# Kernel tuning notes

Measured on AMD Instinct MI355X. Metric: run time of the kernel, lower is better.

The kernel has to match this reference:

```python
import jax, jax.numpy as jnp
import numpy as np

EMBED_DIM = 1024
NUM_HEADS = 16
HEAD_DIM = EMBED_DIM // NUM_HEADS


def setup_inputs() -> dict:
    key = jax.random.key(0)
    ks = jax.random.split(key, 11)
    B, T, C = 2, 2048, EMBED_DIM
    s = 1.0 / np.sqrt(C)  # ~ torch Linear init scale
    inp = {
        "q": jax.random.normal(ks[0], (B, T, C), jnp.float32),
        "k": jax.random.normal(ks[1], (B, T, C), jnp.float32),
        "v": jax.random.normal(ks[2], (B, T, C), jnp.float32),
        "Wq": jax.random.normal(ks[3], (C, C), jnp.float32) * s,
        "bq": jax.random.normal(ks[4], (C,), jnp.float32) * s,
        "Wk": jax.random.normal(ks[5], (C, C), jnp.float32) * s,
        "bk": jax.random.normal(ks[6], (C,), jnp.float32) * s,
        "Wv": jax.random.normal(ks[7], (C, C), jnp.float32) * s,
        "bv": jax.random.normal(ks[8], (C,), jnp.float32) * s,
        "Wo": jax.random.normal(ks[9], (C, C), jnp.float32) * s,
        "bo": jax.random.normal(ks[10], (C,), jnp.float32) * s,
    }
    return inp


def _split_heads(x):
    B, T, C = x.shape
    return x.reshape(B, T, NUM_HEADS, HEAD_DIM).transpose(0, 2, 1, 3)  # [B,H,T,Dh]


def reference(q, k, v, Wq, bq, Wk, bk, Wv, bv, Wo, bo):
    B, Tq, C = q.shape
    # torch Linear: y = x @ W.T + b
    qh = _split_heads(q @ Wq.T + bq)
    kh = _split_heads(k @ Wk.T + bk)
    vh = _split_heads(v @ Wv.T + bv)
    scale = 1.0 / np.sqrt(HEAD_DIM).astype(np.float32)
    logits = jnp.einsum("bhqd,bhkd->bhqk", qh, kh) * scale
    attn = jax.nn.softmax(logits, axis=-1)
    out = jnp.einsum("bhqk,bhkd->bhqd", attn, vh)
    out = out.transpose(0, 2, 1, 3).reshape(B, Tq, C)
    return out @ Wo.T + bo
```

## Files before the change

### kernel.cpp

```cpp
#include <hip/hip_runtime.h>
#include <stdint.h>

#define T_SEQ 2048
#define CDIM 1024
#define NHEAD 16
#define HDIM 64
#define MROWS 4096

typedef unsigned short u16;
typedef __attribute__((ext_vector_type(8))) short bf16x8;
typedef __attribute__((ext_vector_type(4))) float f32x4;
typedef __attribute__((ext_vector_type(16))) float f32x16;
typedef __attribute__((ext_vector_type(4))) unsigned short u16x4;
typedef __attribute__((ext_vector_type(4))) unsigned int uint4v;

#if __has_builtin(__builtin_amdgcn_exp2f)
#define EXP2(x) __builtin_amdgcn_exp2f(x)
#else
#define EXP2(x) exp2f(x)
#endif

__device__ __forceinline__ u16 f2bf(float f) {
  unsigned u = __builtin_bit_cast(unsigned, f);
  u += 0x7fffu + ((u >> 16) & 1u);
  return (u16)(u >> 16);
}

__device__ __forceinline__ unsigned cvt_pk_bf16(float lo, float hi) {
  unsigned r;
  asm("v_cvt_pk_bf16_f32 %0, %1, %2" : "=v"(r) : "v"(lo), "v"(hi));
  return r;
}

__device__ __forceinline__ void pls(unsigned &a, unsigned &b) {
  asm("v_permlane32_swap_b32 %0, %1" : "+v"(a), "+v"(b));
}

__device__ __forceinline__ void gll16(const void* g, void* l) {
  __builtin_amdgcn_global_load_lds((__attribute__((address_space(1))) void*)(g),
                                   (__attribute__((address_space(3))) void*)(l),
                                   16, 0, 0);
}

__device__ __forceinline__ void wg_barrier() {
  asm volatile("" ::: "memory");
  __builtin_amdgcn_s_barrier();
  asm volatile("" ::: "memory");
}

#define WAIT_VM(N) do { __builtin_amdgcn_s_waitcnt(0xF00 | 0x70 | (N)); \
                        asm volatile("" ::: "memory"); } while (0)

__global__ __launch_bounds__(256)
void cvt_all(const float* __restrict__ q, const float* __restrict__ k, const float* __restrict__ v,
             const float* __restrict__ wq, const float* __restrict__ wk,
             const float* __restrict__ wv, const float* __restrict__ wo,
             u16* __restrict__ qb, u16* __restrict__ kb, u16* __restrict__ vb,
             u16* __restrict__ wqb, u16* __restrict__ wkb, u16* __restrict__ wvb, u16* __restrict__ wob) {
  int b = blockIdx.x;
  const float* src; u16* dst; int base;
  if (b < 1536) {
    int s = b >> 9;
    src = (s == 0) ? q : (s == 1) ? k : v;
    dst = (s == 0) ? qb : (s == 1) ? kb : vb;
    base = (b & 511) * 2048;
  } else {
    int s = (b - 1536) >> 7;
    src = (s == 0) ? wq : (s == 1) ? wk : (s == 2) ? wv : wo;
    dst = (s == 0) ? wqb : (s == 1) ? wkb : (s == 2) ? wvb : wob;
    base = ((b - 1536) & 127) * 2048;
  }
#pragma unroll
  for (int j = 0; j < 8; ++j) {
    int i = base + j * 256 + threadIdx.x;
    float4 a = ((const float4*)src)[i];
    u16x4 o = { f2bf(a.x), f2bf(a.y), f2bf(a.z), f2bf(a.w) };
    ((u16x4*)dst)[i] = o;
  }
}


__device__ __forceinline__ void gemm_stage(const u16* Ag, const u16* Bg, u16* Ad, u16* Bd) {
#pragma unroll
  for (int c = 0; c < 4; ++c) {
    gll16(Ag + c * 32 * CDIM, Ad + c * 2048);
    gll16(Bg + c * 32 * CDIM, Bd + c * 2048);
  }
}

__device__ __forceinline__ void gemm_compute(const u16* As, const u16* Bs,
                                             f32x4 (&acc)[4][4],
                                             int wr, int wc, int lg, int lr) {
#pragma unroll
  for (int kk = 0; kk < 2; ++kk) {
    bf16x8 af[4], bfr[4];
#pragma unroll
    for (int f = 0; f < 4; ++f) {
      int ra = wr * 64 + f * 16 + lr;
      af[f]  = *(const bf16x8*)((const char*)As + ra * 128 + ((lg * 16 + kk * 64) ^ ((ra & 7) << 4)));
      int rb = wc * 64 + f * 16 + lr;
      bfr[f] = *(const bf16x8*)((const char*)Bs + rb * 128 + ((lg * 16 + kk * 64) ^ ((rb & 7) << 4)));
    }
#pragma unroll
    for (int i = 0; i < 4; ++i)
#pragma unroll
      for (int j = 0; j < 4; ++j)
        acc[i][j] = __builtin_amdgcn_mfma_f32_16x16x32_bf16(af[i], bfr[j], acc[i][j], 0, 0, 0);
  }
}

#define GEMM_KLOOP(As, Bs, Ad0, Bd0, Ad1, Bd1)                                 \
  gemm_stage(Ag, Bg, Ad0, Bd0);                                                \
  _Pragma("unroll 1")                                                          \
  for (int kt = 0; kt < 16; ++kt) {                                            \
    wg_barrier();                                                              \
    int nt = (kt + 1 < 16) ? kt + 1 : 15;                                      \
    if (kt & 1) gemm_stage(Ag + nt * 64, Bg + nt * 64, Ad0, Bd0);              \
    else        gemm_stage(Ag + nt * 64, Bg + nt * 64, Ad1, Bd1);              \
    WAIT_VM(8);                                                                \
    wg_barrier();                                                              \
    gemm_compute((kt & 1) ? As[1] : As[0], (kt & 1) ? Bs[1] : Bs[0],           \
                 acc, wr, wc, lg, lr);                                         \
  }

__global__ __launch_bounds__(256)
void gemm_qkv(const u16* __restrict__ A0, const u16* __restrict__ A1, const u16* __restrict__ A2,
              const u16* __restrict__ W0, const u16* __restrict__ W1, const u16* __restrict__ W2,
              const float* __restrict__ b0, const float* __restrict__ b1, const float* __restrict__ b2,
              u16* __restrict__ o0, u16* __restrict__ o1, u16* __restrict__ o2,
              float qscale) {
  __shared__ u16 As[2][128 * 64];
  __shared__ u16 Bs[2][128 * 64];
  const int z = blockIdx.z;
  const u16* A   = (z == 0) ? A0 : (z == 1) ? A1 : A2;
  const u16* Bw  = (z == 0) ? W0 : (z == 1) ? W1 : W2;
  const float* bias = (z == 0) ? b0 : (z == 1) ? b1 : b2;
  u16* outp = (z == 0) ? o0 : (z == 1) ? o1 : o2;
  const float scale = (z == 0) ? qscale : 1.0f;

  const int m0 = blockIdx.y * 128;
  const int n0 = blockIdx.x * 128;
  const int tid = threadIdx.x;
  const int w = tid >> 6, l = tid & 63;
  const int wr = w >> 1, wc = w & 1;
  const int lg = l >> 4, lr = l & 15;

  const int row0 = tid >> 3, slot0 = tid & 7;
  const int so = (slot0 ^ (row0 & 7)) << 3;
  const u16* Ag = A  + ((size_t)(m0 + row0)) * CDIM + so;
  const u16* Bg = Bw + ((size_t)(n0 + row0)) * CDIM + so;
  u16* Ad0 = As[0] + w * 512;  u16* Bd0 = Bs[0] + w * 512;
  u16* Ad1 = As[1] + w * 512;  u16* Bd1 = Bs[1] + w * 512;

  f32x4 acc[4][4] = {};

  GEMM_KLOOP(As, Bs, Ad0, Bd0, Ad1, Bd1)

#pragma unroll
  for (int fj = 0; fj < 4; ++fj) {
    int col = n0 + wc * 64 + fj * 16 + lr;
    float bv = bias[col];
    int h = col >> 6, d = col & 63;
#pragma unroll
    for (int fi = 0; fi < 4; ++fi) {
#pragma unroll
      for (int i = 0; i < 4; ++i) {
        int row = m0 + wr * 64 + fi * 16 + lg * 4 + i;
        float val = (acc[fi][fj][i] + bv) * scale;
        int b = row >> 11, t = row & 2047;
        if (z < 2)
          outp[(((size_t)(b * NHEAD + h)) * T_SEQ + t) * HDIM + d] = f2bf(val);
        else
          outp[(((size_t)(b * NHEAD + h)) * HDIM + d) * T_SEQ + t] = f2bf(val);
      }
    }
  }
}

__global__ __launch_bounds__(256)
void gemm_bt0(const u16* __restrict__ A, const u16* __restrict__ Bw,
              const float* __restrict__ bias, float* __restrict__ outp) {
  __shared__ u16 As[2][128 * 64];
  __shared__ u16 Bs[2][128 * 64];
  const int m0 = blockIdx.y * 128;
  const int n0 = blockIdx.x * 128;
  const int tid = threadIdx.x;
  const int w = tid >> 6, l = tid & 63;
  const int wr = w >> 1, wc = w & 1;
  const int lg = l >> 4, lr = l & 15;

  const int row0 = tid >> 3, slot0 = tid & 7;
  const int so = (slot0 ^ (row0 & 7)) << 3;
  const u16* Ag = A  + ((size_t)(m0 + row0)) * CDIM + so;
  const u16* Bg = Bw + ((size_t)(n0 + row0)) * CDIM + so;
  u16* Ad0 = As[0] + w * 512;  u16* Bd0 = Bs[0] + w * 512;
  u16* Ad1 = As[1] + w * 512;  u16* Bd1 = Bs[1] + w * 512;

  f32x4 acc[4][4] = {};

  GEMM_KLOOP(As, Bs, Ad0, Bd0, Ad1, Bd1)

#pragma unroll
  for (int fj = 0; fj < 4; ++fj) {
    int col = n0 + wc * 64 + fj * 16 + lr;
    float bv = bias[col];
#pragma unroll
    for (int fi = 0; fi < 4; ++fi) {
#pragma unroll
      for (int i = 0; i < 4; ++i) {
        int row = m0 + wr * 64 + fi * 16 + lg * 4 + i;
        outp[(size_t)row * CDIM + col] = acc[fi][fj][i] + bv;
      }
    }
  }
}


__device__ __forceinline__ void attn_stage(const u16* Kg, const u16* Vg, u16* Kd, u16* Vd) {
#pragma unroll
  for (int c = 0; c < 2; ++c) {
    gll16(Kg + c * 32 * HDIM,  Kd + c * 2048);
    gll16(Vg + c * 32 * T_SEQ, Vd + c * 2048);
  }
}

__device__ __forceinline__ void attn_tile(const char* Kb, const char* Vb,
                                          const bf16x8 (&qf)[4],
                                          f32x16 (&acc)[2], f32x4& lsum, float& m_run,
                                          int lo5, int hi, int swz) {
  f32x16 s[2] = {};
  const int colK = 16 * hi;
  __builtin_amdgcn_s_setprio(1);
#pragma unroll
  for (int st = 0; st < 4; ++st) {
    bf16x8 k0 = *(const bf16x8*)(Kb + lo5 * 128        + ((32 * st + colK) ^ swz));
    bf16x8 k1 = *(const bf16x8*)(Kb + (lo5 + 32) * 128 + ((32 * st + colK) ^ swz));
    s[0] = __builtin_amdgcn_mfma_f32_32x32x16_bf16(k0, qf[st], s[0], 0, 0, 0);
    s[1] = __builtin_amdgcn_mfma_f32_32x32x16_bf16(k1, qf[st], s[1], 0, 0, 0);
  }
  __builtin_amdgcn_s_setprio(0);

  float t[8];
#pragma unroll
  for (int i = 0; i < 8; ++i)
    t[i] = fmaxf(fmaxf(s[0][2 * i], s[0][2 * i + 1]), fmaxf(s[1][2 * i], s[1][2 * i + 1]));
  float u0 = fmaxf(fmaxf(t[0], t[1]), fmaxf(t[2], t[3]));
  float u1 = fmaxf(fmaxf(t[4], t[5]), fmaxf(t[6], t[7]));
  float tl = fmaxf(u0, u1);
  if (!__all(tl <= m_run + 8.f)) {
    float tmax = fmaxf(tl, __shfl_xor(tl, 32));
    float m_new = fmaxf(m_run, tmax);
    float alpha = EXP2(m_run - m_new);
    lsum[0] *= alpha; lsum[1] *= alpha; lsum[2] *= alpha; lsum[3] *= alpha;
#pragma unroll
    for (int i = 0; i < 16; ++i) { acc[0][i] *= alpha; acc[1][i] *= alpha; }
    m_run = m_new;
  }

  unsigned pg[2][8];
#pragma unroll
  for (int g = 0; g < 8; ++g) {
    float a0 = EXP2(s[0][2 * g] - m_run), b0 = EXP2(s[0][2 * g + 1] - m_run);
    float a1 = EXP2(s[1][2 * g] - m_run), b1 = EXP2(s[1][2 * g + 1] - m_run);
    lsum[g & 3] += (a0 + b0) + (a1 + b1);
    pg[0][g] = cvt_pk_bf16(a0, b0);
    pg[1][g] = cvt_pk_bf16(a1, b1);
  }

  bf16x8 pb[4];
#pragma unroll
  for (int sub = 0; sub < 2; ++sub)
#pragma unroll
    for (int ks = 0; ks < 2; ++ks) {
      unsigned w0 = pg[sub][4 * ks + 0], w1 = pg[sub][4 * ks + 1];
      unsigned w2 = pg[sub][4 * ks + 2], w3 = pg[sub][4 * ks + 3];
      pls(w0, w2); pls(w1, w3);
      uint4v tt = { w0, w1, w2, w3 };
      pb[2 * sub + ks] = __builtin_bit_cast(bf16x8, tt);
    }

  __builtin_amdgcn_s_setprio(1);
#pragma unroll
  for (int ks = 0; ks < 4; ++ks) {
    bf16x8 v0 = *(const bf16x8*)(Vb + lo5 * 128        + ((32 * ks + colK) ^ swz));
    bf16x8 v1 = *(const bf16x8*)(Vb + (lo5 + 32) * 128 + ((32 * ks + colK) ^ swz));
    acc[0] = __builtin_amdgcn_mfma_f32_32x32x16_bf16(v0, pb[ks], acc[0], 0, 0, 0);
    acc[1] = __builtin_amdgcn_mfma_f32_32x32x16_bf16(v1, pb[ks], acc[1], 0, 0, 0);
  }
  __builtin_amdgcn_s_setprio(0);
}

__global__ __launch_bounds__(256)
void attn_fused(const u16* __restrict__ Qh, const u16* __restrict__ Kh,
                const u16* __restrict__ Vt, u16* __restrict__ Ao) {
  __shared__ u16 Ks[2][64 * 64];
  __shared__ u16 Vs[2][64 * 64];
  const int bh = blockIdx.y;
  const int q0 = blockIdx.x * 128;
  const int tid = threadIdx.x;
  const int w = tid >> 6, l = tid & 63;
  const int lo5 = l & 31, hi = l >> 5;
  const int swz = (l & 7) << 4;

  const u16* qptr = Qh + ((size_t)bh * T_SEQ + q0 + w * 32 + lo5) * HDIM + hi * 8;
  bf16x8 qf[4];
#pragma unroll
  for (int s = 0; s < 4; ++s) qf[s] = *(const bf16x8*)(qptr + 16 * s);

  const int row0 = tid >> 3, slot0 = tid & 7;
  const int so = (slot0 ^ (row0 & 7)) << 3;
  const u16* Kg = Kh + ((size_t)bh * T_SEQ + row0) * HDIM + so;
  const u16* Vg = Vt + ((size_t)bh * HDIM + row0) * T_SEQ + so;
  u16* Kd0 = Ks[0] + w * 512;  u16* Vd0 = Vs[0] + w * 512;
  u16* Kd1 = Ks[1] + w * 512;  u16* Vd1 = Vs[1] + w * 512;

  f32x16 acc[2] = {};
  f32x4 lsum = {};
  float m_run = -1e30f;

  attn_stage(Kg, Vg, Kd0, Vd0);
#pragma unroll 1
  for (int kv = 0; kv < 32; ++kv) {
    wg_barrier();
    int nt = (kv + 1 < 32) ? kv + 1 : 31;
    if (kv & 1) attn_stage(Kg + (size_t)nt * 64 * HDIM, Vg + nt * 64, Kd0, Vd0);
    else        attn_stage(Kg + (size_t)nt * 64 * HDIM, Vg + nt * 64, Kd1, Vd1);
    WAIT_VM(4);
    wg_barrier();
    attn_tile((const char*)(kv & 1 ? Ks[1] : Ks[0]),
              (const char*)(kv & 1 ? Vs[1] : Vs[0]),
              qf, acc, lsum, m_run, lo5, hi, swz);
  }

  float ls = (lsum[0] + lsum[1]) + (lsum[2] + lsum[3]);
  ls += __shfl_xor(ls, 32);
  float inv = 1.f / ls;

  wg_barrier();
  char* os = (char*)(Ks[0]) + w * 4096;
#pragma unroll
  for (int dsub = 0; dsub < 2; ++dsub)
#pragma unroll
    for (int gg = 0; gg < 4; ++gg) {
      unsigned wa = cvt_pk_bf16(acc[dsub][4 * gg + 0] * inv, acc[dsub][4 * gg + 1] * inv);
      unsigned wb = cvt_pk_bf16(acc[dsub][4 * gg + 2] * inv, acc[dsub][4 * gg + 3] * inv);
      uint2 wv = { wa, wb };
      int byte = lo5 * 128 + (((32 * dsub + 8 * gg + 4 * hi) * 2) ^ swz);
      *(uint2*)(os + byte) = wv;
    }
  int b = bh >> 4, h = bh & 15;
#pragma unroll
  for (int c = 0; c < 4; ++c) {
    int qq = 8 * c + (l >> 3);
    uint4v ov = *(const uint4v*)(os + qq * 128 + ((16 * (l & 7)) ^ ((qq & 7) << 4)));
    *(uint4v*)(Ao + ((size_t)(b * T_SEQ + q0 + w * 32 + qq)) * CDIM + h * HDIM + (l & 7) * 8) = ov;
  }
}

extern "C" void kernel_launch(void* const* d_in, const int* in_sizes, int n_in,
                              void* d_out, int out_size, void* d_ws, size_t ws_size,
                              hipStream_t stream) {
  const float* q  = (const float*)d_in[0];
  const float* k  = (const float*)d_in[1];
  const float* v  = (const float*)d_in[2];
  const float* Wq = (const float*)d_in[3];
  const float* bq = (const float*)d_in[4];
  const float* Wk = (const float*)d_in[5];
  const float* bk = (const float*)d_in[6];
  const float* Wv = (const float*)d_in[7];
  const float* bv = (const float*)d_in[8];
  const float* Wo = (const float*)d_in[9];
  const float* bo = (const float*)d_in[10];

  char* ws = (char*)d_ws;
  size_t off = 0;
  auto alloc = [&](size_t n) { void* p = ws + off; off += (n + 255) & ~(size_t)255; return p; };
  const size_t NX = (size_t)MROWS * CDIM;
  const size_t NW = (size_t)CDIM * CDIM;
  u16* qb  = (u16*)alloc(NX * 2);
  u16* kb  = (u16*)alloc(NX * 2);
  u16* vb  = (u16*)alloc(NX * 2);
  u16* Wqb = (u16*)alloc(NW * 2);
  u16* Wkb = (u16*)alloc(NW * 2);
  u16* Wvb = (u16*)alloc(NW * 2);
  u16* Wob = (u16*)alloc(NW * 2);
  u16* Qhp = (u16*)alloc(NX * 2);
  u16* Khp = (u16*)alloc(NX * 2);
  u16* Vtp = (u16*)alloc(NX * 2);
  u16* Aop = (u16*)alloc(NX * 2);

  cvt_all<<<2048, 256, 0, stream>>>(q, k, v, Wq, Wk, Wv, Wo,
                                    qb, kb, vb, Wqb, Wkb, Wvb, Wob);

  const float qscale = 0.18033688011112042f;
  gemm_qkv<<<dim3(CDIM / 128, MROWS / 128, 3), 256, 0, stream>>>(
      qb, kb, vb, Wqb, Wkb, Wvb, bq, bk, bv, Qhp, Khp, Vtp, qscale);

  attn_fused<<<dim3(T_SEQ / 128, 32), 256, 0, stream>>>(Qhp, Khp, Vtp, Aop);

  gemm_bt0<<<dim3(CDIM / 128, MROWS / 128), 256, 0, stream>>>(Aop, Wob, bo, (float*)d_out);

  (void)in_sizes; (void)n_in; (void)out_size; (void)ws_size;
}
```

Before: 136.0 us.

## Split attention KV loop across two wave groups with cross-group softmax merge

The attention kernel now launches 512 threads per block, and two groups of four waves each process alternating KV tiles for the same 128 queries. This halves the serial KV iteration count per wave. At the end the partial max, sum and accumulators are merged through shared memory. The change doubles the LDS staging buffers to 64KB and adds an epilogue exchange with extra barriers, which may lower occupancy.

```diff
diff --git a/kernel.cpp b/kernel.cpp
--- a/kernel.cpp
+++ b/kernel.cpp
@@ -216,14 +216,6 @@
 }
 
 
-__device__ __forceinline__ void attn_stage(const u16* Kg, const u16* Vg, u16* Kd, u16* Vd) {
-#pragma unroll
-  for (int c = 0; c < 2; ++c) {
-    gll16(Kg + c * 32 * HDIM,  Kd + c * 2048);
-    gll16(Vg + c * 32 * T_SEQ, Vd + c * 2048);
-  }
-}
-
 __device__ __forceinline__ void attn_tile(const char* Kb, const char* Vb,
                                           const bf16x8 (&qf)[4],
                                           f32x16 (&acc)[2], f32x4& lsum, float& m_run,
@@ -290,70 +282,122 @@
   __builtin_amdgcn_s_setprio(0);
 }
 
-__global__ __launch_bounds__(256)
+__global__ __launch_bounds__(512, 4)
 void attn_fused(const u16* __restrict__ Qh, const u16* __restrict__ Kh,
                 const u16* __restrict__ Vt, u16* __restrict__ Ao) {
-  __shared__ u16 Ks[2][64 * 64];
-  __shared__ u16 Vs[2][64 * 64];
+  __shared__ u16 Ks[2][2][64 * 64];
+  __shared__ u16 Vs[2][2][64 * 64];
   const int bh = blockIdx.y;
   const int q0 = blockIdx.x * 128;
   const int tid = threadIdx.x;
   const int w = tid >> 6, l = tid & 63;
+  const int grp = w >> 2, wq = w & 3;
   const int lo5 = l & 31, hi = l >> 5;
   const int swz = (l & 7) << 4;
 
-  const u16* qptr = Qh + ((size_t)bh * T_SEQ + q0 + w * 32 + lo5) * HDIM + hi * 8;
+  const u16* qptr = Qh + ((size_t)bh * T_SEQ + q0 + wq * 32 + lo5) * HDIM + hi * 8;
   bf16x8 qf[4];
 #pragma unroll
   for (int s = 0; s < 4; ++s) qf[s] = *(const bf16x8*)(qptr + 16 * s);
 
-  const int row0 = tid >> 3, slot0 = tid & 7;
-  const int so = (slot0 ^ (row0 & 7)) << 3;
-  const u16* Kg = Kh + ((size_t)bh * T_SEQ + row0) * HDIM + so;
-  const u16* Vg = Vt + ((size_t)bh * HDIM + row0) * T_SEQ + so;
-  u16* Kd0 = Ks[0] + w * 512;  u16* Vd0 = Vs[0] + w * 512;
-  u16* Kd1 = Ks[1] + w * 512;  u16* Vd1 = Vs[1] + w * 512;
+  const int par = w & 1, sub = (w >> 1) & 1;
+  const int row8 = l >> 3, slot = l & 7;
+
+  auto stage = [&](int step, int db) {
+    int t = 2 * step + par;
+    if (grp == 0) {
+      u16* dst = Ks[db][par] + sub * 32 * 64;
+      const u16* src = Kh + ((size_t)bh * T_SEQ + (size_t)t * 64 + sub * 32 + row8) * HDIM
+                          + ((slot ^ row8) << 3);
+#pragma unroll
+      for (int j = 0; j < 4; ++j)
+        gll16(src + j * 8 * HDIM, dst + j * 8 * 64);
+    } else {
+      u16* dst = Vs[db][par] + sub * 32 * 64;
+      const u16* src = Vt + ((size_t)bh * HDIM + sub * 32 + row8) * T_SEQ + (size_t)t * 64
+                          + ((slot ^ row8) << 3);
+#pragma unroll
+      for (int j = 0; j < 4; ++j)
+        gll16(src + (size_t)j * 8 * T_SEQ, dst + j * 8 * 64);
+    }
+  };
 
   f32x16 acc[2] = {};
   f32x4 lsum = {};
   float m_run = -1e30f;
 
-  attn_stage(Kg, Vg, Kd0, Vd0);
+  stage(0, 0);
 #pragma unroll 1
-  for (int kv = 0; kv < 32; ++kv) {
+  for (int s = 0; s < 16; ++s) {
     wg_barrier();
-    int nt = (kv + 1 < 32) ? kv + 1 : 31;
-    if (kv & 1) attn_stage(Kg + (size_t)nt * 64 * HDIM, Vg + nt * 64, Kd0, Vd0);
-    else        attn_stage(Kg + (size_t)nt * 64 * HDIM, Vg + nt * 64, Kd1, Vd1);
+    int ns = (s + 1 < 16) ? s + 1 : 15;
+    stage(ns, (s + 1) & 1);
     WAIT_VM(4);
     wg_barrier();
-    attn_tile((const char*)(kv & 1 ? Ks[1] : Ks[0]),
-              (const char*)(kv & 1 ? Vs[1] : Vs[0]),
+    attn_tile((const char*)Ks[s & 1][grp], (const char*)Vs[s & 1][grp],
               qf, acc, lsum, m_run, lo5, hi, swz);
   }
 
   float ls = (lsum[0] + lsum[1]) + (lsum[2] + lsum[3]);
   ls += __shfl_xor(ls, 32);
-  float inv = 1.f / ls;
 
   wg_barrier();
-  char* os = (char*)(Ks[0]) + w * 4096;
-#pragma unroll
-  for (int dsub = 0; dsub < 2; ++dsub)
-#pragma unroll
-    for (int gg = 0; gg < 4; ++gg) {
-      unsigned wa = cvt_pk_bf16(acc[dsub][4 * gg + 0] * inv, acc[dsub][4 * gg + 1] * inv);
-      unsigned wb = cvt_pk_bf16(acc[dsub][4 * gg + 2] * inv, acc[dsub][4 * gg + 3] * inv);
-      uint2 wv = { wa, wb };
-      int byte = lo5 * 128 + (((32 * dsub + 8 * gg + 4 * hi) * 2) ^ swz);
-      *(uint2*)(os + byte) = wv;
-    }
-  int b = bh >> 4, h = bh & 15;
-#pragma unroll
-  for (int c = 0; c < 4; ++c) {
-    int qq = 8 * c + (l >> 3);
-    uint4v ov = *(const uint4v*)(os + qq * 128 + ((16 * (l & 7)) ^ ((qq & 7) << 4)));
-    *(uint4v*)(Ao + ((size_t)(b * T_SEQ + q0 + w * 32 + qq)) * CDIM + h * HDIM + (l & 7) * 8) = ov;
+  float* ex = (float*)&Ks[0][0][0];
+  if (hi == 0) {
+    ex[w * 32 + lo5] = m_run;
+    ex[256 + w * 32 + lo5] = ls;
+  }
+  wg_barrier();
+  const int ow = w ^ 4;
+  float m_oth = ex[ow * 32 + lo5];
+  float l_oth = ex[256 + ow * 32 + lo5];
+  float m_fin = fmaxf(m_run, m_oth);
+  float fs = EXP2(m_run - m_fin);
+  float fo = EXP2(m_oth - m_fin);
+  float l_tot = ls * fs + l_oth * fo;
+#pragma unroll
+  for (int i = 0; i < 16; ++i) { acc[0][i] *= fs; acc[1][i] *= fs; }
+
+  float* ab = (float*)&Vs[0][0][0];
+  if (grp == 1) {
+#pragma unroll
+    for (int du = 0; du < 2; ++du)
+#pragma unroll
+      for (int c = 0; c < 4; ++c) {
+        f32x4 t4 = { acc[du][4 * c + 0], acc[du][4 * c + 1],
+                     acc[du][4 * c + 2], acc[du][4 * c + 3] };
+        *(f32x4*)(ab + ((wq * 64 + l) * 32 + du * 16 + c * 4)) = t4;
+      }
+  }
+  wg_barrier();
+  if (grp == 0) {
+#pragma unroll
+    for (int du = 0; du < 2; ++du)
+#pragma unroll
+      for (int c = 0; c < 4; ++c) {
+        f32x4 t4 = *(const f32x4*)(ab + ((wq * 64 + l) * 32 + du * 16 + c * 4));
+        acc[du][4 * c + 0] += t4[0]; acc[du][4 * c + 1] += t4[1];
+        acc[du][4 * c + 2] += t4[2]; acc[du][4 * c + 3] += t4[3];
+      }
+    float inv = 1.f / l_tot;
+    char* os = (char*)&Ks[0][0][0] + 4096 + wq * 4096;
+#pragma unroll
+    for (int dsub = 0; dsub < 2; ++dsub)
+#pragma unroll
+      for (int gg = 0; gg < 4; ++gg) {
+        unsigned wa = cvt_pk_bf16(acc[dsub][4 * gg + 0] * inv, acc[dsub][4 * gg + 1] * inv);
+        unsigned wb = cvt_pk_bf16(acc[dsub][4 * gg + 2] * inv, acc[dsub][4 * gg + 3] * inv);
+        uint2 wv = { wa, wb };
+        int byte = lo5 * 128 + (((32 * dsub + 8 * gg + 4 * hi) * 2) ^ swz);
+        *(uint2*)(os + byte) = wv;
+      }
+    int b = bh >> 4, h = bh & 15;
+#pragma unroll
+    for (int c = 0; c < 4; ++c) {
+      int qq = 8 * c + (l >> 3);
+      uint4v ov = *(const uint4v*)(os + qq * 128 + ((16 * (l & 7)) ^ ((qq & 7) << 4)));
+      *(uint4v*)(Ao + ((size_t)(b * T_SEQ + q0 + wq * 32 + qq)) * CDIM + h * HDIM + (l & 7) * 8) = ov;
+    }
   }
 }
 
@@ -396,7 +440,7 @@
   gemm_qkv<<<dim3(CDIM / 128, MROWS / 128, 3), 256, 0, stream>>>(
       qb, kb, vb, Wqb, Wkb, Wvb, bq, bk, bv, Qhp, Khp, Vtp, qscale);
 
-  attn_fused<<<dim3(T_SEQ / 128, 32), 256, 0, stream>>>(Qhp, Khp, Vtp, Aop);
+  attn_fused<<<dim3(T_SEQ / 128, 32), 512, 0, stream>>>(Qhp, Khp, Vtp, Aop);
 
   gemm_bt0<<<dim3(CDIM / 128, MROWS / 128), 256, 0, stream>>>(Aop, Wob, bo, (float*)d_out);
 
```

Result: faster. 129.2 us (-5.0%).

## Split attention KV range across two blocks and combine partials

Applied to the files above, without the earlier changes.

Splits each attention block's 32 KV tiles into two halves handled by separate blocks (grid z=2), writing partial normalized outputs plus running max and sum, then adds a combine kernel that merges the two halves with softmax rescaling. This doubles the attention grid from 512 to 1024 blocks to improve CU occupancy on the 256-CU device, and sets launch bounds to allow 4 blocks per CU. It also changes the staging so each wave loads either K or V. The cost is an extra kernel launch, extra global traffic for the partials, and partial outputs rounded to bf16 before the combine.

```diff
diff --git a/kernel.cpp b/kernel.cpp
--- a/kernel.cpp
+++ b/kernel.cpp
@@ -24,6 +24,10 @@
   unsigned u = __builtin_bit_cast(unsigned, f);
   u += 0x7fffu + ((u >> 16) & 1u);
   return (u16)(u >> 16);
+}
+
+__device__ __forceinline__ float bf2f(unsigned hw) {
+  return __builtin_bit_cast(float, hw << 16);
 }
 
 __device__ __forceinline__ unsigned cvt_pk_bf16(float lo, float hi) {
@@ -216,14 +220,6 @@
 }
 
 
-__device__ __forceinline__ void attn_stage(const u16* Kg, const u16* Vg, u16* Kd, u16* Vd) {
-#pragma unroll
-  for (int c = 0; c < 2; ++c) {
-    gll16(Kg + c * 32 * HDIM,  Kd + c * 2048);
-    gll16(Vg + c * 32 * T_SEQ, Vd + c * 2048);
-  }
-}
-
 __device__ __forceinline__ void attn_tile(const char* Kb, const char* Vb,
                                           const bf16x8 (&qf)[4],
                                           f32x16 (&acc)[2], f32x4& lsum, float& m_run,
@@ -290,13 +286,15 @@
   __builtin_amdgcn_s_setprio(0);
 }
 
-__global__ __launch_bounds__(256)
+__global__ __launch_bounds__(256, 4)
 void attn_fused(const u16* __restrict__ Qh, const u16* __restrict__ Kh,
-                const u16* __restrict__ Vt, u16* __restrict__ Ao) {
+                const u16* __restrict__ Vt, u16* __restrict__ Op,
+                float2* __restrict__ ml) {
   __shared__ u16 Ks[2][64 * 64];
   __shared__ u16 Vs[2][64 * 64];
   const int bh = blockIdx.y;
   const int q0 = blockIdx.x * 128;
+  const int half = blockIdx.z;
   const int tid = threadIdx.x;
   const int w = tid >> 6, l = tid & 63;
   const int lo5 = l & 31, hi = l >> 5;
@@ -307,28 +305,42 @@
 #pragma unroll
   for (int s = 0; s < 4; ++s) qf[s] = *(const bf16x8*)(qptr + 16 * s);
 
-  const int row0 = tid >> 3, slot0 = tid & 7;
-  const int so = (slot0 ^ (row0 & 7)) << 3;
-  const u16* Kg = Kh + ((size_t)bh * T_SEQ + row0) * HDIM + so;
-  const u16* Vg = Vt + ((size_t)bh * HDIM + row0) * T_SEQ + so;
-  u16* Kd0 = Ks[0] + w * 512;  u16* Vd0 = Vs[0] + w * 512;
-  u16* Kd1 = Ks[1] + w * 512;  u16* Vd1 = Vs[1] + w * 512;
+  const int srow = (w & 1) * 32 + (l >> 3);
+  const int soff = ((l & 7) ^ ((l >> 3) & 7)) << 3;
+  const u16* Kgs = Kh + ((size_t)bh * T_SEQ + srow) * HDIM + soff;
+  const u16* Vgs = Vt + ((size_t)bh * HDIM + srow) * T_SEQ + soff;
+  const int isV = w >> 1;
+
+  auto stage = [&](int t, int db) {
+    if (!isV) {
+      u16* dst = Ks[db] + (w & 1) * 32 * 64;
+      const u16* src = Kgs + (size_t)t * 64 * HDIM;
+#pragma unroll
+      for (int j = 0; j < 4; ++j)
+        gll16(src + j * 8 * HDIM, dst + j * 8 * 64);
+    } else {
+      u16* dst = Vs[db] + (w & 1) * 32 * 64;
+      const u16* src = Vgs + t * 64;
+#pragma unroll
+      for (int j = 0; j < 4; ++j)
+        gll16(src + (size_t)j * 8 * T_SEQ, dst + j * 8 * 64);
+    }
+  };
 
   f32x16 acc[2] = {};
   f32x4 lsum = {};
   float m_run = -1e30f;
-
-  attn_stage(Kg, Vg, Kd0, Vd0);
+  const int tb = half * 16;
+
+  stage(tb, 0);
 #pragma unroll 1
-  for (int kv = 0; kv < 32; ++kv) {
+  for (int s = 0; s < 16; ++s) {
     wg_barrier();
-    int nt = (kv + 1 < 32) ? kv + 1 : 31;
-    if (kv & 1) attn_stage(Kg + (size_t)nt * 64 * HDIM, Vg + nt * 64, Kd0, Vd0);
-    else        attn_stage(Kg + (size_t)nt * 64 * HDIM, Vg + nt * 64, Kd1, Vd1);
+    int ns = (s + 1 < 16) ? s + 1 : 15;
+    stage(tb + ns, (s + 1) & 1);
     WAIT_VM(4);
     wg_barrier();
-    attn_tile((const char*)(kv & 1 ? Ks[1] : Ks[0]),
-              (const char*)(kv & 1 ? Vs[1] : Vs[0]),
+    attn_tile((const char*)Ks[s & 1], (const char*)Vs[s & 1],
               qf, acc, lsum, m_run, lo5, hi, swz);
   }
 
@@ -337,7 +349,7 @@
   float inv = 1.f / ls;
 
   wg_barrier();
-  char* os = (char*)(Ks[0]) + w * 4096;
+  char* os = (char*)&Ks[0][0] + w * 4096;
 #pragma unroll
   for (int dsub = 0; dsub < 2; ++dsub)
 #pragma unroll
@@ -348,12 +360,47 @@
       int byte = lo5 * 128 + (((32 * dsub + 8 * gg + 4 * hi) * 2) ^ swz);
       *(uint2*)(os + byte) = wv;
     }
-  int b = bh >> 4, h = bh & 15;
+  u16* orow = Op + ((size_t)(half * 32 + bh) * T_SEQ + q0 + w * 32) * HDIM;
 #pragma unroll
   for (int c = 0; c < 4; ++c) {
     int qq = 8 * c + (l >> 3);
     uint4v ov = *(const uint4v*)(os + qq * 128 + ((16 * (l & 7)) ^ ((qq & 7) << 4)));
-    *(uint4v*)(Ao + ((size_t)(b * T_SEQ + q0 + w * 32 + qq)) * CDIM + h * HDIM + (l & 7) * 8) = ov;
+    *(uint4v*)(orow + qq * HDIM + (l & 7) * 8) = ov;
+  }
+  if (hi == 0)
+    ml[(size_t)(half * 32 + bh) * T_SEQ + q0 + w * 32 + lo5] = make_float2(m_run, ls);
+}
+
+__global__ __launch_bounds__(256)
+void attn_combine(const u16* __restrict__ Op, const float2* __restrict__ ml,
+                  u16* __restrict__ Ao) {
+  int task0 = blockIdx.x * 256 + threadIdx.x;
+#pragma unroll 1
+  for (int it = 0; it < 4; ++it) {
+    int task = task0 + it * 131072;
+    int chunk = task & 7;
+    int q  = (task >> 3) & 2047;
+    int bh = task >> 14;
+    float2 ml0 = ml[(size_t)bh * T_SEQ + q];
+    float2 ml1 = ml[(size_t)(32 + bh) * T_SEQ + q];
+    float M = fmaxf(ml0.x, ml1.x);
+    float w0 = EXP2(ml0.x - M) * ml0.y;
+    float w1 = EXP2(ml1.x - M) * ml1.y;
+    float zi = 1.f / (w0 + w1);
+    float a0 = w0 * zi, a1 = w1 * zi;
+    const u16* p0 = Op + ((size_t)bh * T_SEQ + q) * HDIM + chunk * 8;
+    const u16* p1 = Op + ((size_t)(32 + bh) * T_SEQ + q) * HDIM + chunk * 8;
+    uint4v o0 = *(const uint4v*)p0;
+    uint4v o1 = *(const uint4v*)p1;
+    uint4v ov;
+#pragma unroll
+    for (int j = 0; j < 4; ++j) {
+      float lo = a0 * bf2f(o0[j] & 0xffffu)  + a1 * bf2f(o1[j] & 0xffffu);
+      float hi = a0 * bf2f(o0[j] >> 16)      + a1 * bf2f(o1[j] >> 16);
+      ov[j] = cvt_pk_bf16(lo, hi);
+    }
+    int b = bh >> 4, h = bh & 15;
+    *(uint4v*)(Ao + ((size_t)(b * T_SEQ + q)) * CDIM + h * HDIM + chunk * 8) = ov;
   }
 }
 
@@ -389,6 +436,9 @@
   u16* Vtp = (u16*)alloc(NX * 2);
   u16* Aop = (u16*)alloc(NX * 2);
 
+  u16* Op = qb;
+  float2* mlp = (float2*)vb;
+
   cvt_all<<<2048, 256, 0, stream>>>(q, k, v, Wq, Wk, Wv, Wo,
                                     qb, kb, vb, Wqb, Wkb, Wvb, Wob);
 
@@ -396,7 +446,8 @@
   gemm_qkv<<<dim3(CDIM / 128, MROWS / 128, 3), 256, 0, stream>>>(
       qb, kb, vb, Wqb, Wkb, Wvb, bq, bk, bv, Qhp, Khp, Vtp, qscale);
 
-  attn_fused<<<dim3(T_SEQ / 128, 32), 256, 0, stream>>>(Qhp, Khp, Vtp, Aop);
+  attn_fused<<<dim3(T_SEQ / 128, 32, 2), 256, 0, stream>>>(Qhp, Khp, Vtp, Op, mlp);
+  attn_combine<<<512, 256, 0, stream>>>(Op, mlp, Aop);
 
   gemm_bt0<<<dim3(CDIM / 128, MROWS / 128), 256, 0, stream>>>(Aop, Wob, bo, (float*)d_out);
 
```

Measured after the change: 132.8 us. 2.4% less time.
